# Optimization experiments

Hardware: AMD Instinct MI355X
Metric: run time of the kernel (lower is better)

## Reference

```python
import jax, jax.numpy as jnp
import numpy as np

N_NODES = 100000
D_IN = 128
D_OUT = 128
B, T, S = 8, 4096, 25


def setup_inputs() -> dict:
    key = jax.random.key(0)
    k1, k2, k3 = jax.random.split(key, 3)
    features = jax.random.normal(k1, (N_NODES, D_IN), dtype=jnp.float32)
    sample_res = jax.random.randint(k2, (B, T, S), 0, N_NODES, dtype=jnp.int64)
    # glorot-uniform init for [D_IN, D_OUT]
    limit = np.sqrt(6.0 / (D_IN + D_OUT)).astype(np.float32)
    weights = jax.random.uniform(k3, (D_IN, D_OUT), dtype=jnp.float32,
                                 minval=-limit, maxval=limit)
    return {"features": features, "sample_res": sample_res, "weights": weights}


def reference(features, sample_res, weights):
    # gather neighbor embeddings: [B, T, S, D]
    sampled = features[sample_res]
    # mean over sampled-neighbor axis -> [B, T, D]
    neigh_vecs = jnp.mean(sampled, axis=2)
    # shared linear transform + relu (bias=False per init defaults)
    out = jnp.einsum('btd,do->bto', neigh_vecs, weights)
    return jax.nn.relu(out)
```

## Files before the change

### kernel.cpp

```cpp
#include <hip/hip_runtime.h>


#define DEG 25
#define DIM 128
#define NPP 25000
#define NPP1 25001

typedef __attribute__((ext_vector_type(8))) short short8;
typedef __attribute__((ext_vector_type(4))) float floatx4;
typedef __attribute__((ext_vector_type(4))) unsigned int uintx4;

__device__ __forceinline__ unsigned short f2bf(float f) {
    unsigned u = __float_as_uint(f);
    return (unsigned short)((u + 0x7fffu + ((u >> 16) & 1u)) >> 16);
}

#define BSTRIDE 136

__global__ __launch_bounds__(256, 2) void gemm_fw(
    const float* __restrict__ A,
    const float* __restrict__ B,
    unsigned short* __restrict__ G,
    int M)
{
    __shared__ unsigned short sBt[DIM * BSTRIDE];

    const int tid = threadIdx.x;

    {
        const float4* B4 = (const float4*)B;
#pragma unroll
        for (int i = 0; i < 16; ++i) {
            const int linear = i * 256 + tid;
            const int k  = linear >> 5;
            const int c4 = linear & 31;
            const float4 v = B4[linear];
            const int n = c4 * 4;
            sBt[(n + 0) * BSTRIDE + k] = f2bf(v.x);
            sBt[(n + 1) * BSTRIDE + k] = f2bf(v.y);
            sBt[(n + 2) * BSTRIDE + k] = f2bf(v.z);
            sBt[(n + 3) * BSTRIDE + k] = f2bf(v.w);
        }
    }
    __syncthreads();

    const int wave = tid >> 6;
    const int lane = tid & 63;
    const int quad = lane >> 4;
    const int l16  = lane & 15;

    const int rw0 = blockIdx.x * 128 + wave * 32;

    floatx4 acc[2][8];
#pragma unroll
    for (int mt = 0; mt < 2; ++mt)
#pragma unroll
        for (int nt = 0; nt < 8; ++nt)
            acc[mt][nt] = (floatx4){0.f, 0.f, 0.f, 0.f};

#pragma unroll
    for (int kt = 0; kt < 4; ++kt) {
        const int k0 = kt * 32;

        short8 afrag[2];
#pragma unroll
        for (int mt = 0; mt < 2; ++mt) {
            int row = rw0 + mt * 16 + l16;
            if (row >= M) row = M - 1;
            const float* ap = A + (size_t)row * DIM + k0 + quad * 8;
            const float4 x = *(const float4*)ap;
            const float4 y = *(const float4*)(ap + 4);
            unsigned p0 = (unsigned)f2bf(x.x) | ((unsigned)f2bf(x.y) << 16);
            unsigned p1 = (unsigned)f2bf(x.z) | ((unsigned)f2bf(x.w) << 16);
            unsigned p2 = (unsigned)f2bf(y.x) | ((unsigned)f2bf(y.y) << 16);
            unsigned p3 = (unsigned)f2bf(y.z) | ((unsigned)f2bf(y.w) << 16);
            uintx4 packed = (uintx4){p0, p1, p2, p3};
            afrag[mt] = __builtin_bit_cast(short8, packed);
        }

#pragma unroll
        for (int nt = 0; nt < 8; ++nt) {
            const uintx4 u = *(const uintx4*)&sBt[(nt * 16 + l16) * BSTRIDE + k0 + quad * 8];
            const short8 bfrag = __builtin_bit_cast(short8, u);
#pragma unroll
            for (int mt = 0; mt < 2; ++mt)
                acc[mt][nt] = __builtin_amdgcn_mfma_f32_16x16x32_bf16(
                    afrag[mt], bfrag, acc[mt][nt], 0, 0, 0);
        }
    }

    __syncthreads();
    {
        unsigned short* sT = sBt + wave * (32 * BSTRIDE);
#pragma unroll
        for (int mt = 0; mt < 2; ++mt)
#pragma unroll
            for (int nt = 0; nt < 8; ++nt)
#pragma unroll
                for (int r = 0; r < 4; ++r)
                    sT[(mt * 16 + quad * 4 + r) * BSTRIDE + nt * 16 + l16] =
                        f2bf(acc[mt][nt][r]);
    }
    __syncthreads();
    {
        const unsigned short* sT = sBt + wave * (32 * BSTRIDE);
        const int oct   = lane & 7;
        const int nrow8 = lane >> 3;
        uintx4* G4 = (uintx4*)G;
#pragma unroll
        for (int g = 0; g < 4; ++g) {
            const int lrow = g * 8 + nrow8;
            const int node = rw0 + lrow;
            if (node < M) {
                const unsigned p     = (unsigned)node / NPP;
                const unsigned local = (unsigned)node - p * NPP;
#pragma unroll
                for (int h = 0; h < 2; ++h) {
                    const uintx4 u = *(const uintx4*)
                        &sT[lrow * BSTRIDE + h * 64 + oct * 8];
                    __builtin_nontemporal_store(u,
                        &G4[((size_t)(p * 2 + h) * NPP1 + local) * 8 + oct]);
                }
            }
        }
        if (blockIdx.x == 0 && tid < 64) {
            const int sl = tid >> 3, o = tid & 7;
            __builtin_nontemporal_store((uintx4){0, 0, 0, 0},
                &G4[((size_t)sl * NPP1 + NPP) * 8 + o]);
        }
    }
}

#define GRB 32

__global__ __launch_bounds__(256, 6) void gather_phased(
    const unsigned short* __restrict__ G,
    const int* __restrict__ idx,
    float* __restrict__ out,
    int n_rows)
{
    __shared__ int sRaw[GRB * DEG];
    __shared__ unsigned short sC[GRB][4][28];
    __shared__ int sCnt[GRB][4];

    const int tid  = threadIdx.x;
    const int h    = blockIdx.x & 1;
    const int rb   = blockIdx.x >> 1;
    const int row0 = rb * GRB;

    const int* ib = idx + (size_t)row0 * DEG;
    for (int i = tid; i < GRB * DEG; i += 256)
        sRaw[i] = __builtin_nontemporal_load(ib + i);
    __syncthreads();

    if (tid < GRB * 4) {
        const int row = tid >> 2;
        const int rg  = tid & 3;
        const int lo  = rg * NPP;
        unsigned short* dst = &sC[row][rg][0];
        int cnt = 0;
#pragma unroll
        for (int s = 0; s < DEG; ++s) {
            const unsigned d = (unsigned)(sRaw[row * DEG + s] - lo);
            if (d < NPP) dst[cnt++] = (unsigned short)d;
        }
        int m = ((cnt + 3) / 4) * 4;
        if (m == 0) m = 4;
        for (int i = cnt; i < m; ++i) dst[i] = (unsigned short)NPP;
        sCnt[row][rg] = m;
    }
    __syncthreads();

    const int oct = tid & 7;
    const int r   = tid >> 3;

    float a0 = 0.f, a1 = 0.f, a2 = 0.f, a3 = 0.f;
    float a4 = 0.f, a5 = 0.f, a6 = 0.f, a7 = 0.f;

#define ACC8(v)                                 \
    do {                                        \
        a0 += __uint_as_float((v).x << 16);     \
        a1 += __uint_as_float((v).x & 0xffff0000u); \
        a2 += __uint_as_float((v).y << 16);     \
        a3 += __uint_as_float((v).y & 0xffff0000u); \
        a4 += __uint_as_float((v).z << 16);     \
        a5 += __uint_as_float((v).z & 0xffff0000u); \
        a6 += __uint_as_float((v).w << 16);     \
        a7 += __uint_as_float((v).w & 0xffff0000u); \
    } while (0)

    for (int p = 0; p < 4; ++p) {
        const uintx4* __restrict__ Gc =
            (const uintx4*)G + (size_t)(p * 2 + h) * NPP1 * 8 + oct;
        const unsigned short* lp = &sC[r][p][0];
        const int m = sCnt[r][p];

        uintx4 v0 = Gc[(size_t)lp[0] * 8];
        uintx4 v1 = Gc[(size_t)lp[1] * 8];
        uintx4 v2 = Gc[(size_t)lp[2] * 8];
        uintx4 v3 = Gc[(size_t)lp[3] * 8];
        for (int i = 4; i < m; i += 4) {
            const uintx4 w0 = Gc[(size_t)lp[i + 0] * 8];
            const uintx4 w1 = Gc[(size_t)lp[i + 1] * 8];
            const uintx4 w2 = Gc[(size_t)lp[i + 2] * 8];
            const uintx4 w3 = Gc[(size_t)lp[i + 3] * 8];
            ACC8(v0); ACC8(v1); ACC8(v2); ACC8(v3);
            v0 = w0; v1 = w1; v2 = w2; v3 = w3;
        }
        ACC8(v0); ACC8(v1); ACC8(v2); ACC8(v3);
    }
#undef ACC8

    const float inv = 1.0f / 25.0f;
    floatx4* op = (floatx4*)(out + (size_t)(row0 + r) * DIM + h * 64 + oct * 8);
    const floatx4 o0 = {fmaxf(a0 * inv, 0.f), fmaxf(a1 * inv, 0.f),
                        fmaxf(a2 * inv, 0.f), fmaxf(a3 * inv, 0.f)};
    const floatx4 o1 = {fmaxf(a4 * inv, 0.f), fmaxf(a5 * inv, 0.f),
                        fmaxf(a6 * inv, 0.f), fmaxf(a7 * inv, 0.f)};
    __builtin_nontemporal_store(o0, op);
    __builtin_nontemporal_store(o1, op + 1);
}

#define RPB 16
#define CG 32

__device__ __forceinline__ float4 relu4(float4 v) {
    return make_float4(fmaxf(v.x, 0.f), fmaxf(v.y, 0.f),
                       fmaxf(v.z, 0.f), fmaxf(v.w, 0.f));
}

__global__ __launch_bounds__(256, 4) void gcn_fused(
    const float* __restrict__ F, const int* __restrict__ idx,
    const float* __restrict__ W, float* __restrict__ out, int n_rows)
{
    __shared__ float4 sV[RPB * CG];
    __shared__ int    sIdx[RPB * DEG];

    const float4* F4 = (const float4*)F;
    const float4* W4 = (const float4*)W;
    float4* out4 = (float4*)out;

    const int tid = threadIdx.x;
    const int row0 = blockIdx.x * RPB;

    for (int i = tid; i < RPB * DEG; i += 256)
        sIdx[i] = idx[(size_t)row0 * DEG + i];
    __syncthreads();

    const int cg = tid & 31;
    const int rs = tid >> 5;

#pragma unroll
    for (int rr = 0; rr < 2; ++rr) {
        const int r = rs + rr * 8;
        int j[DEG];
#pragma unroll
        for (int s = 0; s < DEG; ++s) j[s] = sIdx[r * DEG + s];
        float4 acc = make_float4(0.f, 0.f, 0.f, 0.f);
#pragma unroll
        for (int s = 0; s < DEG; ++s) {
            float4 f = F4[(size_t)j[s] * CG + cg];
            acc.x += f.x; acc.y += f.y; acc.z += f.z; acc.w += f.w;
        }
        const float inv = 1.0f / 25.0f;
        acc.x *= inv; acc.y *= inv; acc.z *= inv; acc.w *= inv;
        sV[r * CG + cg] = acc;
    }
    __syncthreads();

    const float4* vA = &sV[rs * CG];
    const float4* vB = &sV[(rs + 8) * CG];
    float4 o0 = make_float4(0.f, 0.f, 0.f, 0.f);
    float4 o1 = make_float4(0.f, 0.f, 0.f, 0.f);
#pragma unroll 4
    for (int d4 = 0; d4 < CG; ++d4) {
        const float4 a = vA[d4];
        const float4 b = vB[d4];
        const float4 w0 = W4[(size_t)(4 * d4 + 0) * CG + cg];
        const float4 w1 = W4[(size_t)(4 * d4 + 1) * CG + cg];
        const float4 w2 = W4[(size_t)(4 * d4 + 2) * CG + cg];
        const float4 w3 = W4[(size_t)(4 * d4 + 3) * CG + cg];
        o0.x += a.x*w0.x + a.y*w1.x + a.z*w2.x + a.w*w3.x;
        o0.y += a.x*w0.y + a.y*w1.y + a.z*w2.y + a.w*w3.y;
        o0.z += a.x*w0.z + a.y*w1.z + a.z*w2.z + a.w*w3.z;
        o0.w += a.x*w0.w + a.y*w1.w + a.z*w2.w + a.w*w3.w;
        o1.x += b.x*w0.x + b.y*w1.x + b.z*w2.x + b.w*w3.x;
        o1.y += b.x*w0.y + b.y*w1.y + b.z*w2.y + b.w*w3.y;
        o1.z += b.x*w0.z + b.y*w1.z + b.z*w2.z + b.w*w3.z;
        o1.w += b.x*w0.w + b.y*w1.w + b.z*w2.w + b.w*w3.w;
    }
    out4[(size_t)(row0 + rs) * CG + cg]     = relu4(o0);
    out4[(size_t)(row0 + rs + 8) * CG + cg] = relu4(o1);
}

extern "C" void kernel_launch(void* const* d_in, const int* in_sizes, int n_in,
                              void* d_out, int out_size, void* d_ws, size_t ws_size,
                              hipStream_t stream) {
    const float* F   = (const float*)d_in[0];
    const int*   idx = (const int*)d_in[1];
    const float* W   = (const float*)d_in[2];
    float* out = (float*)d_out;

    const int n_nodes = in_sizes[0] / DIM;
    const int n_rows  = in_sizes[1] / DEG;

    const size_t need = (size_t)8 * NPP1 * 64 * sizeof(unsigned short);

    if (n_nodes == 100000 && ws_size >= need && (n_rows & (GRB - 1)) == 0) {
        unsigned short* G = (unsigned short*)d_ws;
        gemm_fw<<<(n_nodes + 127) / 128, 256, 0, stream>>>(F, W, G, n_nodes);
        gather_phased<<<(n_rows / GRB) * 2, 256, 0, stream>>>(G, idx, out, n_rows);
    } else {
        gcn_fused<<<n_rows / RPB, 256, 0, stream>>>(F, idx, W, out, n_rows);
    }
}
```

Baseline: 129.5 us.

## Issue all 25 gathers at once in gather kernel, drop padded zero rows

The gather kernel no longer walks the four node partitions in sequence, each padded to a multiple of four loads. It now builds a compact list of 25 absolute offsets per row, sorted by partition, and issues all 25 16-byte loads up front before accumulating. This removes the padding loads, the zero sentinel row and the per-partition loop overhead, and gives more memory-level parallelism per thread. In exchange each thread holds 25 vector registers, so the occupancy hint is lowered from 6 to 4 blocks per CU, which may reduce latency hiding across waves.

Result: slower. 132.5 us (+2.3%).

```diff
diff --git a/kernel.cpp b/kernel.cpp
--- a/kernel.cpp
+++ b/kernel.cpp
@@ -4,7 +4,6 @@
 #define DEG 25
 #define DIM 128
 #define NPP 25000
-#define NPP1 25001
 
 typedef __attribute__((ext_vector_type(8))) short short8;
 typedef __attribute__((ext_vector_type(4))) float floatx4;
@@ -119,28 +118,23 @@
                     const uintx4 u = *(const uintx4*)
                         &sT[lrow * BSTRIDE + h * 64 + oct * 8];
                     __builtin_nontemporal_store(u,
-                        &G4[((size_t)(p * 2 + h) * NPP1 + local) * 8 + oct]);
+                        &G4[((size_t)(p * 2 + h) * NPP + local) * 8 + oct]);
                 }
             }
         }
-        if (blockIdx.x == 0 && tid < 64) {
-            const int sl = tid >> 3, o = tid & 7;
-            __builtin_nontemporal_store((uintx4){0, 0, 0, 0},
-                &G4[((size_t)sl * NPP1 + NPP) * 8 + o]);
-        }
     }
 }
 
 #define GRB 32
 
-__global__ __launch_bounds__(256, 6) void gather_phased(
+__global__ __launch_bounds__(256, 4) void gather_phased(
     const unsigned short* __restrict__ G,
     const int* __restrict__ idx,
     float* __restrict__ out,
     int n_rows)
 {
     __shared__ int sRaw[GRB * DEG];
-    __shared__ unsigned short sC[GRB][4][28];
+    __shared__ int sOrd[GRB][DEG];
     __shared__ int sCnt[GRB][4];
 
     const int tid  = threadIdx.x;
@@ -157,59 +151,54 @@
         const int row = tid >> 2;
         const int rg  = tid & 3;
         const int lo  = rg * NPP;
-        unsigned short* dst = &sC[row][rg][0];
         int cnt = 0;
 #pragma unroll
         for (int s = 0; s < DEG; ++s) {
             const unsigned d = (unsigned)(sRaw[row * DEG + s] - lo);
-            if (d < NPP) dst[cnt++] = (unsigned short)d;
-        }
-        int m = ((cnt + 3) / 4) * 4;
-        if (m == 0) m = 4;
-        for (int i = cnt; i < m; ++i) dst[i] = (unsigned short)NPP;
-        sCnt[row][rg] = m;
+            cnt += (d < NPP) ? 1 : 0;
+        }
+        sCnt[row][rg] = cnt;
+    }
+    __syncthreads();
+
+    if (tid < GRB * 4) {
+        const int row = tid >> 2;
+        const int rg  = tid & 3;
+        const int lo  = rg * NPP;
+        int off = 0;
+        for (int q = 0; q < 4; ++q) off += (q < rg) ? sCnt[row][q] : 0;
+        const int base = (rg * 2 + h) * NPP - lo;
+#pragma unroll
+        for (int s = 0; s < DEG; ++s) {
+            const int raw = sRaw[row * DEG + s];
+            const unsigned d = (unsigned)(raw - lo);
+            if (d < NPP) sOrd[row][off++] = raw + base;
+        }
     }
     __syncthreads();
 
     const int oct = tid & 7;
     const int r   = tid >> 3;
+    const uintx4* __restrict__ G4 = (const uintx4*)G + oct;
+
+    uintx4 v[DEG];
+#pragma unroll
+    for (int s = 0; s < DEG; ++s)
+        v[s] = G4[(size_t)sOrd[r][s] * 8];
 
     float a0 = 0.f, a1 = 0.f, a2 = 0.f, a3 = 0.f;
     float a4 = 0.f, a5 = 0.f, a6 = 0.f, a7 = 0.f;
-
-#define ACC8(v)                                 \
-    do {                                        \
-        a0 += __uint_as_float((v).x << 16);     \
-        a1 += __uint_as_float((v).x & 0xffff0000u); \
-        a2 += __uint_as_float((v).y << 16);     \
-        a3 += __uint_as_float((v).y & 0xffff0000u); \
-        a4 += __uint_as_float((v).z << 16);     \
-        a5 += __uint_as_float((v).z & 0xffff0000u); \
-        a6 += __uint_as_float((v).w << 16);     \
-        a7 += __uint_as_float((v).w & 0xffff0000u); \
-    } while (0)
-
-    for (int p = 0; p < 4; ++p) {
-        const uintx4* __restrict__ Gc =
-            (const uintx4*)G + (size_t)(p * 2 + h) * NPP1 * 8 + oct;
-        const unsigned short* lp = &sC[r][p][0];
-        const int m = sCnt[r][p];
-
-        uintx4 v0 = Gc[(size_t)lp[0] * 8];
-        uintx4 v1 = Gc[(size_t)lp[1] * 8];
-        uintx4 v2 = Gc[(size_t)lp[2] * 8];
-        uintx4 v3 = Gc[(size_t)lp[3] * 8];
-        for (int i = 4; i < m; i += 4) {
-            const uintx4 w0 = Gc[(size_t)lp[i + 0] * 8];
-            const uintx4 w1 = Gc[(size_t)lp[i + 1] * 8];
-            const uintx4 w2 = Gc[(size_t)lp[i + 2] * 8];
-            const uintx4 w3 = Gc[(size_t)lp[i + 3] * 8];
-            ACC8(v0); ACC8(v1); ACC8(v2); ACC8(v3);
-            v0 = w0; v1 = w1; v2 = w2; v3 = w3;
-        }
-        ACC8(v0); ACC8(v1); ACC8(v2); ACC8(v3);
-    }
-#undef ACC8
+#pragma unroll
+    for (int s = 0; s < DEG; ++s) {
+        a0 += __uint_as_float(v[s].x << 16);
+        a1 += __uint_as_float(v[s].x & 0xffff0000u);
+        a2 += __uint_as_float(v[s].y << 16);
+        a3 += __uint_as_float(v[s].y & 0xffff0000u);
+        a4 += __uint_as_float(v[s].z << 16);
+        a5 += __uint_as_float(v[s].z & 0xffff0000u);
+        a6 += __uint_as_float(v[s].w << 16);
+        a7 += __uint_as_float(v[s].w & 0xffff0000u);
+    }
 
     const float inv = 1.0f / 25.0f;
     floatx4* op = (floatx4*)(out + (size_t)(row0 + r) * DIM + h * 64 + oct * 8);
@@ -304,7 +293,7 @@
     const int n_nodes = in_sizes[0] / DIM;
     const int n_rows  = in_sizes[1] / DEG;
 
-    const size_t need = (size_t)8 * NPP1 * 64 * sizeof(unsigned short);
+    const size_t need = (size_t)8 * NPP * 64 * sizeof(unsigned short);
 
     if (n_nodes == 100000 && ws_size >= need && (n_rows & (GRB - 1)) == 0) {
         unsigned short* G = (unsigned short*)d_ws;
```
